# Kernel optimization log

Hardware: AMD Instinct MI355X
Metric: run time of the kernel (lower is better)

Reference implementation:

```python
import jax, jax.numpy as jnp
import numpy as np

N_NODES = 50000


def gcn_conv(x, edge_index, W, b, n):
    # PyG GCNConv: xW, add self-loops, symmetric degree normalization,
    # scatter-add messages from source (row) to target (col).
    xw = x @ W
    row, col = edge_index[0], edge_index[1]
    loops = jnp.arange(n, dtype=edge_index.dtype)
    row = jnp.concatenate([row, loops])
    col = jnp.concatenate([col, loops])
    deg = jax.ops.segment_sum(jnp.ones(row.shape[0], dtype=xw.dtype), col, num_segments=n)
    dinv = jnp.where(deg > 0, jax.lax.rsqrt(deg), 0.0)
    norm = dinv[row] * dinv[col]  # [E+N]
    out = jax.ops.segment_sum(xw[row] * norm[:, None], col, num_segments=n)
    return out + b


def setup_inputs() -> dict:
    key = jax.random.key(0)
    ks = jax.random.split(key, 5)
    n, d_in, d_h, d_out, n_edges = N_NODES, 128, 128, 4, 600000
    x = jax.random.normal(ks[0], (n, d_in), dtype=jnp.float32)
    edge_index = jax.random.randint(ks[1], (2, n_edges), 0, n, dtype=jnp.int64)
    W1 = jax.random.normal(ks[2], (d_in, d_h), dtype=jnp.float32) * (1.0 / np.sqrt(d_in))
    b1 = jnp.zeros((d_h,), dtype=jnp.float32)
    W2 = jax.random.normal(ks[3], (d_h, d_h), dtype=jnp.float32) * (1.0 / np.sqrt(d_h))
    b2 = jnp.zeros((d_h,), dtype=jnp.float32)
    Wfc = jax.random.normal(ks[4], (2 * d_h, d_out), dtype=jnp.float32) * (1.0 / np.sqrt(2 * d_h))
    bfc = jnp.zeros((d_out,), dtype=jnp.float32)
    return {"x": x, "edge_index": edge_index, "W1": W1, "b1": b1,
            "W2": W2, "b2": b2, "Wfc": Wfc, "bfc": bfc}


def reference(x, edge_index, W1, b1, W2, b2, Wfc, bfc):
    n = x.shape[0]
    # dropout is identity at inference (training=False)
    h = jax.nn.relu(gcn_conv(x, edge_index, W1, b1, n))
    h = jax.nn.relu(gcn_conv(h, edge_index, W2, b2, n))
    # edge-level gather + concat + linear classifier
    edge_x = jnp.concatenate([h[edge_index[0]], h[edge_index[1]]], axis=-1)  # [E, 2*d_h]
    edge_scores = edge_x @ Wfc + bfc  # [E, d_out]
    return jax.nn.log_softmax(edge_scores, axis=1)
```

## Files before the change

### kernel.cpp

```cpp
#include <hip/hip_runtime.h>
#include <math.h>
#include <stdint.h>

#define D 128
#define SCAN_CHUNK 2048
#define LDA 136

typedef __attribute__((ext_vector_type(8))) short v8s;
typedef __attribute__((ext_vector_type(4))) float v4f;

static __device__ __forceinline__ uint16_t f2bf(float f) {
    uint32_t u = __float_as_uint(f);
    u = (u + 0x7fff + ((u >> 16) & 1)) >> 16;
    return (uint16_t)u;
}
static __device__ __forceinline__ float bf2f(uint16_t h) { return __uint_as_float((uint32_t)h << 16); }
static __device__ __forceinline__ float bf_lo(uint32_t u) { return __uint_as_float(u << 16); }
static __device__ __forceinline__ float bf_hi(uint32_t u) { return __uint_as_float(u & 0xffff0000u); }


__global__ void countpack_kernel(const int* __restrict__ col, int* __restrict__ cnt, int E,
                                 const float* __restrict__ W1, const float* __restrict__ W2,
                                 uint16_t* __restrict__ Wh, uint16_t* __restrict__ Wl) {
    int tid = blockIdx.x * blockDim.x + threadIdx.x;
    if (tid < 2 * 16384) {
        int layer = tid >> 14;
        int li = tid & 16383;
        int j = li & 7, lane = (li >> 3) & 63, f = li >> 9;
        int kstep = f >> 3, tile = f & 7;
        int k = kstep * 32 + ((lane >> 4) * 8) + j;
        int nn = tile * 16 + (lane & 15);
        const float* W = layer ? W2 : W1;
        float v = W[k * 128 + nn];
        uint16_t h = f2bf(v);
        Wh[tid] = h;
        Wl[tid] = f2bf(v - bf2f(h));
    }
    if (tid < E) atomicAdd(&cnt[col[tid]], 1);
}


__global__ __launch_bounds__(256) void scanA_kernel(const int* __restrict__ cnt,
                                                    int* __restrict__ bsum,
                                                    float* __restrict__ dinv, int n) {
    __shared__ int wsum[4];
    int b = blockIdx.x, t = threadIdx.x;
    int base = b * SCAN_CHUNK;
    int s = 0;
#pragma unroll
    for (int k = 0; k < SCAN_CHUNK / 256; k++) {
        int i = base + k * 256 + t;
        if (i < n) {
            int c = cnt[i];
            s += c;
            dinv[i] = rsqrtf((float)c + 1.0f);
        }
    }
#pragma unroll
    for (int off = 32; off > 0; off >>= 1) s += __shfl_xor(s, off, 64);
    if ((t & 63) == 0) wsum[t >> 6] = s;
    __syncthreads();
    if (t == 0) bsum[b] = wsum[0] + wsum[1] + wsum[2] + wsum[3];
}


__global__ __launch_bounds__(256) void scanC_kernel(const int* __restrict__ cnt,
                                                    const int* __restrict__ bsum,
                                                    int* __restrict__ offs, int n, int nb) {
    __shared__ int stage[SCAN_CHUNK];
    __shared__ int res[SCAN_CHUNK];
    __shared__ int tsum[256];
    __shared__ int sb[64];
    int b = blockIdx.x, t = threadIdx.x;
    if (t < 64) {
        int v = (t < nb) ? bsum[t] : 0;
        int inc = v;
#pragma unroll
        for (int off = 1; off < 64; off <<= 1) {
            int u = __shfl_up(inc, off, 64);
            if (t >= off) inc += u;
        }
        sb[t] = inc;
    }
    int base = b * SCAN_CHUNK;
#pragma unroll
    for (int k = 0; k < SCAN_CHUNK / 256; k++) {
        int i = base + k * 256 + t;
        stage[k * 256 + t] = (i < n) ? cnt[i] : 0;
    }
    __syncthreads();
    int my = 0;
#pragma unroll
    for (int j = 0; j < 8; j++) my += stage[t * 8 + j];
    tsum[t] = my;
    __syncthreads();
    for (int off = 1; off < 256; off <<= 1) {
        int v = (t >= off) ? tsum[t - off] : 0;
        __syncthreads();
        tsum[t] += v;
        __syncthreads();
    }
    int bbase = (b == 0) ? 0 : sb[b - 1];
    int run = tsum[t] - my + bbase;
#pragma unroll
    for (int j = 0; j < 8; j++) {
        res[t * 8 + j] = run;
        run += stage[t * 8 + j];
    }
    __syncthreads();
#pragma unroll
    for (int k = 0; k < SCAN_CHUNK / 256; k++) {
        int i = base + k * 256 + t;
        if (i < n) offs[i] = res[k * 256 + t];
    }
    if (b == gridDim.x - 1 && t == 0) offs[n] = sb[nb - 1];
}

__global__ void fill_kernel(const int* row, const int* col, const int* offs,
                            int* curs, int* adj, int E) {
    int e = blockIdx.x * blockDim.x + threadIdx.x;
    if (e < E) {
        int c = col[e];
        int p = atomicAdd(&curs[c], 1);
        adj[offs[c] + p] = row[e];
    }
}


__global__ __launch_bounds__(256) void gemm_mfma_kernel(const float* __restrict__ A,
                                                        const uint16_t* __restrict__ Wph,
                                                        const uint16_t* __restrict__ Wpl,
                                                        const float* __restrict__ dinv,
                                                        uint16_t* __restrict__ Cb, int M) {
    __shared__ uint16_t Ah[64][LDA];
    __shared__ uint16_t Al[64][LDA];
    int t = threadIdx.x;
    int base_row = blockIdx.x * 64;

#pragma unroll
    for (int kk = 0; kk < 8; kk++) {
        int idx = kk * 256 + t;
        int r = idx >> 5;
        int c4 = idx & 31;
        int gr = base_row + r;
        float4 f = (gr < M) ? *(const float4*)(A + (size_t)gr * D + c4 * 4)
                            : make_float4(0.f, 0.f, 0.f, 0.f);
        uint16_t h0 = f2bf(f.x), h1 = f2bf(f.y), h2 = f2bf(f.z), h3 = f2bf(f.w);
        uint16_t l0 = f2bf(f.x - bf2f(h0)), l1 = f2bf(f.y - bf2f(h1));
        uint16_t l2 = f2bf(f.z - bf2f(h2)), l3 = f2bf(f.w - bf2f(h3));
        *(ushort4*)&Ah[r][c4 * 4] = make_ushort4(h0, h1, h2, h3);
        *(ushort4*)&Al[r][c4 * 4] = make_ushort4(l0, l1, l2, l3);
    }
    __syncthreads();

    int lane = t & 63, w = t >> 6;
    int m_l = lane & 15, quad = lane >> 4;
    int arow = w * 16 + m_l;

    v4f acc[8];
#pragma unroll
    for (int i = 0; i < 8; i++) acc[i] = (v4f){0.f, 0.f, 0.f, 0.f};

#pragma unroll
    for (int ks = 0; ks < 4; ks++) {
        v8s ah = *(const v8s*)&Ah[arow][ks * 32 + quad * 8];
        v8s al = *(const v8s*)&Al[arow][ks * 32 + quad * 8];
#pragma unroll
        for (int ti = 0; ti < 8; ti++) {
            int f = ks * 8 + ti;
            v8s bh = *(const v8s*)(Wph + ((size_t)(f * 64 + lane)) * 8);
            v8s bl = *(const v8s*)(Wpl + ((size_t)(f * 64 + lane)) * 8);
            acc[ti] = __builtin_amdgcn_mfma_f32_16x16x32_bf16(al, bh, acc[ti], 0, 0, 0);
            acc[ti] = __builtin_amdgcn_mfma_f32_16x16x32_bf16(ah, bl, acc[ti], 0, 0, 0);
            acc[ti] = __builtin_amdgcn_mfma_f32_16x16x32_bf16(ah, bh, acc[ti], 0, 0, 0);
        }
    }

    int rbase = base_row + w * 16 + quad * 4;
#pragma unroll
    for (int reg = 0; reg < 4; reg++) {
        int gr = rbase + reg;
        if (gr < M) {
            float di = dinv[gr];
#pragma unroll
            for (int ti = 0; ti < 8; ti++) {
                Cb[(size_t)gr * D + ti * 16 + m_l] = f2bf(di * acc[ti][reg]);
            }
        }
    }
}


__global__ __launch_bounds__(256) void agg_kernel(const uint32_t* __restrict__ xwb,
                                                  const int* __restrict__ adj,
                                                  const int* __restrict__ offs,
                                                  const float* __restrict__ dinv,
                                                  const float* __restrict__ bias,
                                                  float* __restrict__ hout, int n) {
    int wave = (int)((blockIdx.x * (size_t)blockDim.x + threadIdx.x) >> 6);
    int lane = threadIdx.x & 63;
    if (wave >= n) return;
    int i = wave;
    uint32_t su = xwb[(size_t)i * (D / 2) + lane];
    float acc0 = bf_lo(su);
    float acc1 = bf_hi(su);
    int s = offs[i], e = offs[i + 1];
    int j = s;
    for (; j + 7 < e; j += 8) {
        int r0 = adj[j],     r1 = adj[j + 1], r2 = adj[j + 2], r3 = adj[j + 3];
        int r4 = adj[j + 4], r5 = adj[j + 5], r6 = adj[j + 6], r7 = adj[j + 7];
        uint32_t u0 = xwb[(size_t)r0 * (D / 2) + lane];
        uint32_t u1 = xwb[(size_t)r1 * (D / 2) + lane];
        uint32_t u2 = xwb[(size_t)r2 * (D / 2) + lane];
        uint32_t u3 = xwb[(size_t)r3 * (D / 2) + lane];
        uint32_t u4 = xwb[(size_t)r4 * (D / 2) + lane];
        uint32_t u5 = xwb[(size_t)r5 * (D / 2) + lane];
        uint32_t u6 = xwb[(size_t)r6 * (D / 2) + lane];
        uint32_t u7 = xwb[(size_t)r7 * (D / 2) + lane];
        acc0 += bf_lo(u0); acc1 += bf_hi(u0);
        acc0 += bf_lo(u1); acc1 += bf_hi(u1);
        acc0 += bf_lo(u2); acc1 += bf_hi(u2);
        acc0 += bf_lo(u3); acc1 += bf_hi(u3);
        acc0 += bf_lo(u4); acc1 += bf_hi(u4);
        acc0 += bf_lo(u5); acc1 += bf_hi(u5);
        acc0 += bf_lo(u6); acc1 += bf_hi(u6);
        acc0 += bf_lo(u7); acc1 += bf_hi(u7);
    }
    for (; j + 3 < e; j += 4) {
        int r0 = adj[j], r1 = adj[j + 1], r2 = adj[j + 2], r3 = adj[j + 3];
        uint32_t u0 = xwb[(size_t)r0 * (D / 2) + lane];
        uint32_t u1 = xwb[(size_t)r1 * (D / 2) + lane];
        uint32_t u2 = xwb[(size_t)r2 * (D / 2) + lane];
        uint32_t u3 = xwb[(size_t)r3 * (D / 2) + lane];
        acc0 += bf_lo(u0); acc1 += bf_hi(u0);
        acc0 += bf_lo(u1); acc1 += bf_hi(u1);
        acc0 += bf_lo(u2); acc1 += bf_hi(u2);
        acc0 += bf_lo(u3); acc1 += bf_hi(u3);
    }
    for (; j < e; j++) {
        int r = adj[j];
        uint32_t u = xwb[(size_t)r * (D / 2) + lane];
        acc0 += bf_lo(u); acc1 += bf_hi(u);
    }
    float di = dinv[i];
    float2 bv = ((const float2*)bias)[lane];
    float o0 = fmaxf(fmaf(di, acc0, bv.x), 0.f);
    float o1 = fmaxf(fmaf(di, acc1, bv.y), 0.f);
    ((float2*)(hout + (size_t)i * D))[lane] = make_float2(o0, o1);
}


__global__ __launch_bounds__(256) void pq_kernel(const float* __restrict__ h,
                                                 const float* __restrict__ Wfc,
                                                 const float* __restrict__ bfc,
                                                 float* __restrict__ P1,
                                                 float* __restrict__ P2, int n) {
    int i = blockIdx.x * blockDim.x + threadIdx.x;
    if (i >= n) return;
    const float4* hr = (const float4*)(h + (size_t)i * D);
    const float4* W4 = (const float4*)Wfc;
    float p0 = bfc[0], p1 = bfc[1], p2 = bfc[2], p3 = bfc[3];
    float q0 = 0.f, q1 = 0.f, q2 = 0.f, q3 = 0.f;
#pragma unroll 8
    for (int kk = 0; kk < 32; kk++) {
        float4 f = hr[kk];
#pragma unroll
        for (int j = 0; j < 4; j++) {
            float fv = (j == 0) ? f.x : (j == 1) ? f.y : (j == 2) ? f.z : f.w;
            int k = kk * 4 + j;
            float4 w1 = W4[k];
            float4 w2 = W4[128 + k];
            p0 = fmaf(fv, w1.x, p0); p1 = fmaf(fv, w1.y, p1);
            p2 = fmaf(fv, w1.z, p2); p3 = fmaf(fv, w1.w, p3);
            q0 = fmaf(fv, w2.x, q0); q1 = fmaf(fv, w2.y, q1);
            q2 = fmaf(fv, w2.z, q2); q3 = fmaf(fv, w2.w, q3);
        }
    }
    ((float4*)P1)[i] = make_float4(p0, p1, p2, p3);
    ((float4*)P2)[i] = make_float4(q0, q1, q2, q3);
}


__global__ __launch_bounds__(256) void edge2_kernel(const int* __restrict__ row,
                                                    const int* __restrict__ col,
                                                    const float* __restrict__ P1,
                                                    const float* __restrict__ P2,
                                                    float* __restrict__ out, int E) {
    int e = blockIdx.x * blockDim.x + threadIdx.x;
    if (e >= E) return;
    int r = row[e], c = col[e];
    float4 a = ((const float4*)P1)[r];
    float4 b = ((const float4*)P2)[c];
    float sx = a.x + b.x, sy = a.y + b.y, sz = a.z + b.z, sw = a.w + b.w;
    float m = fmaxf(fmaxf(sx, sy), fmaxf(sz, sw));
    float e0 = expf(sx - m), e1 = expf(sy - m), e2 = expf(sz - m), e3 = expf(sw - m);
    float lse = m + logf(e0 + e1 + e2 + e3);
    *(float4*)(out + (size_t)e * 4) = make_float4(sx - lse, sy - lse, sz - lse, sw - lse);
}


extern "C" void kernel_launch(void* const* d_in, const int* in_sizes, int n_in,
                              void* d_out, int out_size, void* d_ws, size_t ws_size,
                              hipStream_t stream) {
    const float* x   = (const float*)d_in[0];
    const int*   ei  = (const int*)d_in[1];
    const float* W1  = (const float*)d_in[2];
    const float* b1  = (const float*)d_in[3];
    const float* W2  = (const float*)d_in[4];
    const float* b2  = (const float*)d_in[5];
    const float* Wfc = (const float*)d_in[6];
    const float* bfc = (const float*)d_in[7];
    float* out = (float*)d_out;

    int n = in_sizes[0] / D;
    int E = in_sizes[1] / 2;
    const int* row = ei;
    const int* col = ei + E;

    int nbScan = (n + SCAN_CHUNK - 1) / SCAN_CHUNK;

    uint16_t* xwb  = (uint16_t*)d_ws;
    float*    h    = (float*)(xwb + (size_t)n * D);
    int*      cnt  = (int*)(h + (size_t)n * D);
    int*      curs = cnt + n;
    int*      offs = curs + n;
    int*      bsum = offs + (n + 4);
    int*      adj  = bsum + 64;
    float*    dinv = (float*)(adj + E);
    uint16_t* Wph  = (uint16_t*)(dinv + n);
    uint16_t* Wpl  = Wph + 2 * 16384;
    float*    P1   = (float*)(Wpl + 2 * 16384);
    float*    P2   = P1 + (size_t)n * 4;

    int nb_n = (n + 255) / 256;
    int nb_e = (E + 255) / 256;

    hipMemsetAsync(cnt, 0, (size_t)2 * n * sizeof(int), stream);
    countpack_kernel<<<nb_e, 256, 0, stream>>>(col, cnt, E, W1, W2, Wph, Wpl);
    scanA_kernel<<<nbScan, 256, 0, stream>>>(cnt, bsum, dinv, n);
    scanC_kernel<<<nbScan, 256, 0, stream>>>(cnt, bsum, offs, n, nbScan);
    fill_kernel<<<nb_e, 256, 0, stream>>>(row, col, offs, curs, adj, E);

    int nbG = (n + 63) / 64;

    gemm_mfma_kernel<<<nbG, 256, 0, stream>>>(x, Wph, Wpl, dinv, xwb, n);
    agg_kernel<<<(n + 3) / 4, 256, 0, stream>>>((const uint32_t*)xwb, adj, offs, dinv, b1, h, n);
    gemm_mfma_kernel<<<nbG, 256, 0, stream>>>(h, Wph + 16384, Wpl + 16384, dinv, xwb, n);
    agg_kernel<<<(n + 3) / 4, 256, 0, stream>>>((const uint32_t*)xwb, adj, offs, dinv, b2, h, n);

    pq_kernel<<<nb_n, 256, 0, stream>>>(h, Wfc, bfc, P1, P2, n);
    edge2_kernel<<<nb_e, 256, 0, stream>>>(row, col, P1, P2, out, E);
}
```

Baseline: 258.6 us.

## Fuse second aggregation with edge-classifier projection and reuse count atomics for CSR fill

```diff
diff --git a/kernel.cpp b/kernel.cpp
--- a/kernel.cpp
+++ b/kernel.cpp
@@ -19,7 +19,8 @@
 static __device__ __forceinline__ float bf_hi(uint32_t u) { return __uint_as_float(u & 0xffff0000u); }
 
 
-__global__ void countpack_kernel(const int* __restrict__ col, int* __restrict__ cnt, int E,
+__global__ void countpack_kernel(const int* __restrict__ col, int* __restrict__ cnt,
+                                 int* __restrict__ rnk, int E,
                                  const float* __restrict__ W1, const float* __restrict__ W2,
                                  uint16_t* __restrict__ Wh, uint16_t* __restrict__ Wl) {
     int tid = blockIdx.x * blockDim.x + threadIdx.x;
@@ -36,7 +37,7 @@
         Wh[tid] = h;
         Wl[tid] = f2bf(v - bf2f(h));
     }
-    if (tid < E) atomicAdd(&cnt[col[tid]], 1);
+    if (tid < E) rnk[tid] = atomicAdd(&cnt[col[tid]], 1);
 }
 
 
@@ -116,14 +117,12 @@
     if (b == gridDim.x - 1 && t == 0) offs[n] = sb[nb - 1];
 }
 
-__global__ void fill_kernel(const int* row, const int* col, const int* offs,
-                            int* curs, int* adj, int E) {
+
+__global__ void fill_kernel(const int* __restrict__ row, const int* __restrict__ col,
+                            const int* __restrict__ rnk, const int* __restrict__ offs,
+                            int* __restrict__ adj, int E) {
     int e = blockIdx.x * blockDim.x + threadIdx.x;
-    if (e < E) {
-        int c = col[e];
-        int p = atomicAdd(&curs[c], 1);
-        adj[offs[c] + p] = row[e];
-    }
+    if (e < E) adj[offs[col[e]] + rnk[e]] = row[e];
 }
 
 
@@ -250,34 +249,90 @@
 }
 
 
-__global__ __launch_bounds__(256) void pq_kernel(const float* __restrict__ h,
-                                                 const float* __restrict__ Wfc,
-                                                 const float* __restrict__ bfc,
-                                                 float* __restrict__ P1,
-                                                 float* __restrict__ P2, int n) {
-    int i = blockIdx.x * blockDim.x + threadIdx.x;
-    if (i >= n) return;
-    const float4* hr = (const float4*)(h + (size_t)i * D);
+__global__ __launch_bounds__(256) void agg2pq_kernel(const uint32_t* __restrict__ xwb,
+                                                     const int* __restrict__ adj,
+                                                     const int* __restrict__ offs,
+                                                     const float* __restrict__ dinv,
+                                                     const float* __restrict__ bias,
+                                                     const float* __restrict__ Wfc,
+                                                     const float* __restrict__ bfc,
+                                                     float* __restrict__ P1,
+                                                     float* __restrict__ P2, int n) {
+    int wave = (int)((blockIdx.x * (size_t)blockDim.x + threadIdx.x) >> 6);
+    int lane = threadIdx.x & 63;
+    if (wave >= n) return;
+    int i = wave;
+    uint32_t su = xwb[(size_t)i * (D / 2) + lane];
+    float acc0 = bf_lo(su);
+    float acc1 = bf_hi(su);
+    int s = offs[i], e = offs[i + 1];
+    int j = s;
+    for (; j + 7 < e; j += 8) {
+        int r0 = adj[j],     r1 = adj[j + 1], r2 = adj[j + 2], r3 = adj[j + 3];
+        int r4 = adj[j + 4], r5 = adj[j + 5], r6 = adj[j + 6], r7 = adj[j + 7];
+        uint32_t u0 = xwb[(size_t)r0 * (D / 2) + lane];
+        uint32_t u1 = xwb[(size_t)r1 * (D / 2) + lane];
+        uint32_t u2 = xwb[(size_t)r2 * (D / 2) + lane];
+        uint32_t u3 = xwb[(size_t)r3 * (D / 2) + lane];
+        uint32_t u4 = xwb[(size_t)r4 * (D / 2) + lane];
+        uint32_t u5 = xwb[(size_t)r5 * (D / 2) + lane];
+        uint32_t u6 = xwb[(size_t)r6 * (D / 2) + lane];
+        uint32_t u7 = xwb[(size_t)r7 * (D / 2) + lane];
+        acc0 += bf_lo(u0); acc1 += bf_hi(u0);
+        acc0 += bf_lo(u1); acc1 += bf_hi(u1);
+        acc0 += bf_lo(u2); acc1 += bf_hi(u2);
+        acc0 += bf_lo(u3); acc1 += bf_hi(u3);
+        acc0 += bf_lo(u4); acc1 += bf_hi(u4);
+        acc0 += bf_lo(u5); acc1 += bf_hi(u5);
+        acc0 += bf_lo(u6); acc1 += bf_hi(u6);
+        acc0 += bf_lo(u7); acc1 += bf_hi(u7);
+    }
+    for (; j + 3 < e; j += 4) {
+        int r0 = adj[j], r1 = adj[j + 1], r2 = adj[j + 2], r3 = adj[j + 3];
+        uint32_t u0 = xwb[(size_t)r0 * (D / 2) + lane];
+        uint32_t u1 = xwb[(size_t)r1 * (D / 2) + lane];
+        uint32_t u2 = xwb[(size_t)r2 * (D / 2) + lane];
+        uint32_t u3 = xwb[(size_t)r3 * (D / 2) + lane];
+        acc0 += bf_lo(u0); acc1 += bf_hi(u0);
+        acc0 += bf_lo(u1); acc1 += bf_hi(u1);
+        acc0 += bf_lo(u2); acc1 += bf_hi(u2);
+        acc0 += bf_lo(u3); acc1 += bf_hi(u3);
+    }
+    for (; j < e; j++) {
+        int r = adj[j];
+        uint32_t u = xwb[(size_t)r * (D / 2) + lane];
+        acc0 += bf_lo(u); acc1 += bf_hi(u);
+    }
+    float di = dinv[i];
+    float2 bv = ((const float2*)bias)[lane];
+    float o0 = fmaxf(fmaf(di, acc0, bv.x), 0.f);
+    float o1 = fmaxf(fmaf(di, acc1, bv.y), 0.f);
+
     const float4* W4 = (const float4*)Wfc;
-    float p0 = bfc[0], p1 = bfc[1], p2 = bfc[2], p3 = bfc[3];
-    float q0 = 0.f, q1 = 0.f, q2 = 0.f, q3 = 0.f;
-#pragma unroll 8
-    for (int kk = 0; kk < 32; kk++) {
-        float4 f = hr[kk];
-#pragma unroll
-        for (int j = 0; j < 4; j++) {
-            float fv = (j == 0) ? f.x : (j == 1) ? f.y : (j == 2) ? f.z : f.w;
-            int k = kk * 4 + j;
-            float4 w1 = W4[k];
-            float4 w2 = W4[128 + k];
-            p0 = fmaf(fv, w1.x, p0); p1 = fmaf(fv, w1.y, p1);
-            p2 = fmaf(fv, w1.z, p2); p3 = fmaf(fv, w1.w, p3);
-            q0 = fmaf(fv, w2.x, q0); q1 = fmaf(fv, w2.y, q1);
-            q2 = fmaf(fv, w2.z, q2); q3 = fmaf(fv, w2.w, q3);
-        }
-    }
-    ((float4*)P1)[i] = make_float4(p0, p1, p2, p3);
-    ((float4*)P2)[i] = make_float4(q0, q1, q2, q3);
+    float4 wa = W4[2 * lane];
+    float4 wb = W4[2 * lane + 1];
+    float4 wc = W4[128 + 2 * lane];
+    float4 wd = W4[129 + 2 * lane];
+    float p0 = fmaf(o0, wa.x, o1 * wb.x), p1 = fmaf(o0, wa.y, o1 * wb.y);
+    float p2 = fmaf(o0, wa.z, o1 * wb.z), p3 = fmaf(o0, wa.w, o1 * wb.w);
+    float q0 = fmaf(o0, wc.x, o1 * wd.x), q1 = fmaf(o0, wc.y, o1 * wd.y);
+    float q2 = fmaf(o0, wc.z, o1 * wd.z), q3 = fmaf(o0, wc.w, o1 * wd.w);
+#pragma unroll
+    for (int off = 1; off < 64; off <<= 1) {
+        p0 += __shfl_xor(p0, off, 64);
+        p1 += __shfl_xor(p1, off, 64);
+        p2 += __shfl_xor(p2, off, 64);
+        p3 += __shfl_xor(p3, off, 64);
+        q0 += __shfl_xor(q0, off, 64);
+        q1 += __shfl_xor(q1, off, 64);
+        q2 += __shfl_xor(q2, off, 64);
+        q3 += __shfl_xor(q3, off, 64);
+    }
+    if (lane == 0) {
+        float4 bb = *(const float4*)bfc;
+        *(float4*)(P1 + (size_t)i * 4) = make_float4(p0 + bb.x, p1 + bb.y, p2 + bb.z, p3 + bb.w);
+        *(float4*)(P2 + (size_t)i * 4) = make_float4(q0, q1, q2, q3);
+    }
 }
 
 
@@ -322,32 +377,31 @@
     uint16_t* xwb  = (uint16_t*)d_ws;
     float*    h    = (float*)(xwb + (size_t)n * D);
     int*      cnt  = (int*)(h + (size_t)n * D);
-    int*      curs = cnt + n;
-    int*      offs = curs + n;
+    int*      offs = cnt + n;
     int*      bsum = offs + (n + 4);
     int*      adj  = bsum + 64;
-    float*    dinv = (float*)(adj + E);
+    int*      rnk  = adj + E;
+    float*    dinv = (float*)(rnk + E);
     uint16_t* Wph  = (uint16_t*)(dinv + n);
     uint16_t* Wpl  = Wph + 2 * 16384;
     float*    P1   = (float*)(Wpl + 2 * 16384);
     float*    P2   = P1 + (size_t)n * 4;
 
-    int nb_n = (n + 255) / 256;
     int nb_e = (E + 255) / 256;
 
-    hipMemsetAsync(cnt, 0, (size_t)2 * n * sizeof(int), stream);
-    countpack_kernel<<<nb_e, 256, 0, stream>>>(col, cnt, E, W1, W2, Wph, Wpl);
+    hipMemsetAsync(cnt, 0, (size_t)n * sizeof(int), stream);
+    countpack_kernel<<<nb_e, 256, 0, stream>>>(col, cnt, rnk, E, W1, W2, Wph, Wpl);
     scanA_kernel<<<nbScan, 256, 0, stream>>>(cnt, bsum, dinv, n);
     scanC_kernel<<<nbScan, 256, 0, stream>>>(cnt, bsum, offs, n, nbScan);
-    fill_kernel<<<nb_e, 256, 0, stream>>>(row, col, offs, curs, adj, E);
+    fill_kernel<<<nb_e, 256, 0, stream>>>(row, col, rnk, offs, adj, E);
 
     int nbG = (n + 63) / 64;
 
     gemm_mfma_kernel<<<nbG, 256, 0, stream>>>(x, Wph, Wpl, dinv, xwb, n);
     agg_kernel<<<(n + 3) / 4, 256, 0, stream>>>((const uint32_t*)xwb, adj, offs, dinv, b1, h, n);
     gemm_mfma_kernel<<<nbG, 256, 0, stream>>>(h, Wph + 16384, Wpl + 16384, dinv, xwb, n);
-    agg_kernel<<<(n + 3) / 4, 256, 0, stream>>>((const uint32_t*)xwb, adj, offs, dinv, b2, h, n);
-
-    pq_kernel<<<nb_n, 256, 0, stream>>>(h, Wfc, bfc, P1, P2, n);
+    agg2pq_kernel<<<(n + 3) / 4, 256, 0, stream>>>((const uint32_t*)xwb, adj, offs, dinv, b2,
+                                                   Wfc, bfc, P1, P2, n);
+
     edge2_kernel<<<nb_e, 256, 0, stream>>>(row, col, P1, P2, out, E);
 }
```

Result: faster. 236.7 us (-8.5%).
